# Performance work log

Measured on AMD Instinct MI355X. Metric: run time of the kernel, lower is better.

The kernel has to match this reference:

```python
import jax, jax.numpy as jnp
import numpy as np

B, T, D, H, F = 256, 128, 64, 512, 256


def setup_inputs() -> dict:
    key = jax.random.key(0)
    ks = jax.random.split(key, 4)
    return {
        "observations": jax.random.normal(ks[0], (B, T, D), dtype=jnp.float32),
        "Wx": jax.random.normal(ks[1], (D, 4 * H), dtype=jnp.float32) / np.sqrt(D),
        "Wh": jax.random.normal(ks[2], (H, 4 * H), dtype=jnp.float32) / np.sqrt(H),
        "b": jnp.zeros((4 * H,), dtype=jnp.float32),
        "Wd": jax.random.normal(ks[3], (H, F), dtype=jnp.float32) / np.sqrt(H),
        "bd": jnp.zeros((F,), dtype=jnp.float32),
    }


def reference(observations, Wx, Wh, b, Wd, bd):
    # observations: [B, T, D]. Flax nnx.LSTMCell gate order: i, f, g, o;
    # input kernels have no bias, hidden kernels carry the bias.
    batch = observations.shape[0]
    hidden = Wh.shape[0]
    # Precompute input projections for all timesteps in one big GEMM: [T, B, 4H]
    x_proj = jnp.einsum("btd,dg->tbg", observations, Wx)

    def step(carry, xp_t):
        c, h = carry
        gates = xp_t + h @ Wh + b  # [B, 4H]
        i, f, g, o = jnp.split(gates, 4, axis=-1)
        i = jax.nn.sigmoid(i)
        f = jax.nn.sigmoid(f)
        g = jnp.tanh(g)
        o = jax.nn.sigmoid(o)
        c_new = f * c + i * g
        h_new = o * jnp.tanh(c_new)
        return (c_new, h_new), None

    c0 = jnp.zeros((batch, hidden), dtype=observations.dtype)
    h0 = jnp.zeros((batch, hidden), dtype=observations.dtype)
    (c_last, h_last), _ = jax.lax.scan(step, (c0, h0), x_proj)
    return jax.nn.relu(h_last @ Wd + bd)
```

## Files before the change

### kernel.cpp

```cpp
#include <hip/hip_runtime.h>


#define WH_S 524
#define WX_S 72
#define HT_S 524

typedef __attribute__((ext_vector_type(4))) _Float16 f16x4;
typedef __attribute__((ext_vector_type(4))) float    f32x4;
typedef __attribute__((ext_vector_type(2))) unsigned long long u64x2;
typedef unsigned long long u64;

__device__ __forceinline__ float sigm(float x)  { return 1.f / (1.f + __expf(-x)); }
__device__ __forceinline__ float tanh_(float x) { float e = __expf(2.f * x); return 1.f - 2.f / (e + 1.f); }

__device__ __forceinline__ u64x2 ld128_cc(const void* p) {
    u64x2 v;
    asm volatile("global_load_dwordx4 %0, %1, off sc0 sc1" : "=v"(v) : "v"(p));
    return v;
}

#define MFMA16(w, a, c) __builtin_amdgcn_mfma_f32_16x16x16f16((w), (a), (c), 0, 0, 0)

__launch_bounds__(256, 1)
__global__ void lstm_persist(const float* __restrict__ obs,
                             const float* __restrict__ Wx,
                             const float* __restrict__ Wh,
                             const float* __restrict__ bvec,
                             u64* __restrict__ hbuf,
                             unsigned* __restrict__ bar)
{
    __shared__ _Float16 sbuf[128 * WH_S];

    const int tid = threadIdx.x, lane = tid & 63, wid = tid >> 6;
    const int grp = blockIdx.x & 15, slc = blockIdx.x >> 4;
    const int l15 = lane & 15, l16 = lane >> 4;
    const int c0 = (wid << 5) + l15, c1 = c0 + 16;

    for (int idx = tid; idx < 512 * 128; idx += 256) {
        int k = idx >> 7, c = idx & 127;
        int u = ((c >> 5) << 3) | (c & 7);
        int g = (((c >> 4) & 1) << 1) | ((c >> 3) & 1);
        sbuf[c * WH_S + k] = (_Float16)Wh[k * 2048 + (g << 9) + (slc << 5) + u];
    }
    __syncthreads();
    f16x4 wf0[32], wf1[32];
    #pragma unroll
    for (int kk = 0; kk < 32; ++kk) {
        wf0[kk] = *(const f16x4*)&sbuf[c0 * WH_S + (kk << 4) + (l16 << 2)];
        wf1[kk] = *(const f16x4*)&sbuf[c1 * WH_S + (kk << 4) + (l16 << 2)];
    }
    __syncthreads();
    for (int idx = tid; idx < 64 * 128; idx += 256) {
        int k = idx >> 7, c = idx & 127;
        int u = ((c >> 5) << 3) | (c & 7);
        int g = (((c >> 4) & 1) << 1) | ((c >> 3) & 1);
        sbuf[c * WX_S + k] = (_Float16)Wx[k * 2048 + (g << 9) + (slc << 5) + u];
    }
    __syncthreads();
    f16x4 xw0[4], xw1[4];
    #pragma unroll
    for (int kx = 0; kx < 4; ++kx) {
        xw0[kx] = *(const f16x4*)&sbuf[c0 * WX_S + (kx << 4) + (l16 << 2)];
        xw1[kx] = *(const f16x4*)&sbuf[c1 * WX_S + (kx << 4) + (l16 << 2)];
    }
    __syncthreads();
    _Float16* const sh = sbuf;

    const int brow = (grp << 4) + l15;
    const int ub   = (wid << 3) + ((l16 & 1) << 2);
    f32x4 bia[4];
    #pragma unroll
    for (int g = 0; g < 4; ++g)
        bia[g] = *(const f32x4*)(bvec + (g << 9) + (slc << 5) + ub);

    const int r_ld  = (wid << 2) + (lane >> 4);
    const int ch16  = lane & 15;
    const int hstore_idx = (brow << 7) + (slc << 3) + (wid << 1) + (l16 & 1);
    unsigned* const ctr = bar + (grp << 4);

    float c_reg[4] = {0.f, 0.f, 0.f, 0.f};

    for (int t = 0; t < 128; ++t) {
        const u64* hc = hbuf + ((t & 1) ? 32768 : 0);
        u64*       hn = hbuf + ((t & 1) ? 0 : 32768);

        const u64* hrow = hc + (((grp << 4) + r_ld) << 7) + (ch16 << 1);
        u64x2 hv4[4];
        #pragma unroll
        for (int j = 0; j < 4; ++j) hv4[j] = ld128_cc(hrow + (j << 5));

        f16x4 xf[4];
        const float* op = obs + ((brow << 7) + t) * 64;
        #pragma unroll
        for (int kx = 0; kx < 4; ++kx) {
            f32x4 ov = *(const f32x4*)(op + (kx << 4) + (l16 << 2));
            #pragma unroll
            for (int e = 0; e < 4; ++e) xf[kx][e] = (_Float16)ov[e];
        }

        asm volatile("s_waitcnt vmcnt(0)" ::: "memory");
        #pragma unroll
        for (int j = 0; j < 4; ++j) {
            *(u64*)&sh[r_ld * HT_S + (j << 7) + (ch16 << 3)]     = hv4[j][0];
            *(u64*)&sh[r_ld * HT_S + (j << 7) + (ch16 << 3) + 4] = hv4[j][1];
        }
        __syncthreads();

        f32x4 a00 = {0.f,0.f,0.f,0.f}, a01 = {0.f,0.f,0.f,0.f};
        f32x4 a10 = {0.f,0.f,0.f,0.f}, a11 = {0.f,0.f,0.f,0.f};

        #pragma unroll
        for (int kx = 0; kx < 4; ++kx) {
            if (kx & 1) { a01 = MFMA16(xw0[kx], xf[kx], a01); a11 = MFMA16(xw1[kx], xf[kx], a11); }
            else        { a00 = MFMA16(xw0[kx], xf[kx], a00); a10 = MFMA16(xw1[kx], xf[kx], a10); }
        }
        #pragma unroll
        for (int kk = 0; kk < 32; ++kk) {
            f16x4 af = *(const f16x4*)&sh[l15 * HT_S + (kk << 4) + (l16 << 2)];
            if (kk & 1) { a01 = MFMA16(wf0[kk], af, a01); a11 = MFMA16(wf1[kk], af, a11); }
            else        { a00 = MFMA16(wf0[kk], af, a00); a10 = MFMA16(wf1[kk], af, a10); }
        }
        f32x4 t0 = a00 + a01, t1 = a10 + a11;

        f32x4 r0, r1;
        #pragma unroll
        for (int rr = 0; rr < 4; ++rr) {
            r0[rr] = __shfl_xor(t0[rr], 32, 64);
            r1[rr] = __shfl_xor(t1[rr], 32, 64);
        }
        const bool low = (l16 < 2);
        f16x4 hv;
        #pragma unroll
        for (int rr = 0; rr < 4; ++rr) {
            float I  = low ? t0[rr] : r0[rr];
            float Fv = low ? r0[rr] : t0[rr];
            float G  = low ? t1[rr] : r1[rr];
            float O  = low ? r1[rr] : t1[rr];
            I  = sigm (I  + bia[0][rr]);
            Fv = sigm (Fv + bia[1][rr]);
            G  = tanh_(G  + bia[2][rr]);
            O  = sigm (O  + bia[3][rr]);
            float cn  = Fv * c_reg[rr] + I * G;
            c_reg[rr] = cn;
            hv[rr] = (_Float16)(O * tanh_(cn));
        }
        if (low)
            __hip_atomic_store(hn + hstore_idx, __builtin_bit_cast(u64, hv),
                               __ATOMIC_RELAXED, __HIP_MEMORY_SCOPE_AGENT);

        if (t < 127) {
            asm volatile("s_waitcnt vmcnt(0)" ::: "memory");
            __syncthreads();
            if (tid == 0) {
                __hip_atomic_fetch_add(ctr, 1u, __ATOMIC_RELAXED, __HIP_MEMORY_SCOPE_AGENT);
                const unsigned tgt = (unsigned)((t + 1) << 4);
                while (__hip_atomic_load(ctr, __ATOMIC_RELAXED, __HIP_MEMORY_SCOPE_AGENT) < tgt)
                    __builtin_amdgcn_s_sleep(1);
            }
            __syncthreads();
        }
    }
}

__launch_bounds__(256)
__global__ void final_proj(const _Float16* __restrict__ hlast,
                           const float* __restrict__ Wd,
                           const float* __restrict__ bd,
                           float* __restrict__ out)
{
    __shared__ float shm[2048];
    const int tid = threadIdx.x;
    const int rb  = blockIdx.x;
    for (int idx = tid; idx < 2048; idx += 256)
        shm[idx] = (float)hlast[(rb << 2) * 512 + idx];
    __syncthreads();
    float a0 = 0.f, a1 = 0.f, a2 = 0.f, a3 = 0.f;
    for (int k = 0; k < 512; ++k) {
        float w = Wd[(k << 8) + tid];
        a0 += shm[k] * w; a1 += shm[512 + k] * w; a2 += shm[1024 + k] * w; a3 += shm[1536 + k] * w;
    }
    float bb = bd[tid];
    float v0 = a0 + bb, v1 = a1 + bb, v2 = a2 + bb, v3 = a3 + bb;
    out[((rb << 2) + 0) * 256 + tid] = v0 > 0.f ? v0 : 0.f;
    out[((rb << 2) + 1) * 256 + tid] = v1 > 0.f ? v1 : 0.f;
    out[((rb << 2) + 2) * 256 + tid] = v2 > 0.f ? v2 : 0.f;
    out[((rb << 2) + 3) * 256 + tid] = v3 > 0.f ? v3 : 0.f;
}

extern "C" void kernel_launch(void* const* d_in, const int* in_sizes, int n_in,
                              void* d_out, int out_size, void* d_ws, size_t ws_size,
                              hipStream_t stream)
{
    (void)in_sizes; (void)n_in; (void)out_size; (void)ws_size;
    const float* obs = (const float*)d_in[0];
    const float* Wx  = (const float*)d_in[1];
    const float* Wh  = (const float*)d_in[2];
    const float* bv  = (const float*)d_in[3];
    const float* Wd  = (const float*)d_in[4];
    const float* bd  = (const float*)d_in[5];
    float* out = (float*)d_out;

    u64* hbuf     = (u64*)d_ws;
    unsigned* bar = (unsigned*)((char*)d_ws + 524288);

    hipMemsetAsync(d_ws, 0, 524288 + 1024, stream);

    void* args[6];
    args[0] = (void*)&obs; args[1] = (void*)&Wx; args[2] = (void*)&Wh;
    args[3] = (void*)&bv;  args[4] = (void*)&hbuf; args[5] = (void*)&bar;
    hipError_t e = hipLaunchCooperativeKernel((const void*)lstm_persist,
                                              dim3(256), dim3(256), args, 0, stream);
    if (e != hipSuccess) {
        lstm_persist<<<dim3(256), dim3(256), 0, stream>>>(obs, Wx, Wh, bv, hbuf, bar);
    }
    final_proj<<<dim3(64), dim3(256), 0, stream>>>((const _Float16*)d_ws, Wd, bd, out);
}
```

Measured before the change: 551.0 us.

## Replace per-group barrier counter with step-tagged hidden-state words polled by consumers

Drops the atomic counter barrier between timesteps. Each fp16 hidden value is now stored in a 32-bit word together with a 16-bit timestep tag, and consumers spin-load their rows until every tag matches the expected step. Blocks then wait only for the data they need instead of a full group arrive-and-wait, and one block-wide sync per step is removed. In exchange the hidden buffer doubles in size, so global traffic and the memset grow, and the design relies on each 128-bit store becoming visible as a unit.

```diff
diff --git a/kernel.cpp b/kernel.cpp
--- a/kernel.cpp
+++ b/kernel.cpp
@@ -7,16 +7,19 @@
 
 typedef __attribute__((ext_vector_type(4))) _Float16 f16x4;
 typedef __attribute__((ext_vector_type(4))) float    f32x4;
-typedef __attribute__((ext_vector_type(2))) unsigned long long u64x2;
-typedef unsigned long long u64;
+typedef __attribute__((ext_vector_type(4))) unsigned u32x4;
+typedef __attribute__((ext_vector_type(2))) unsigned u32x2;
 
 __device__ __forceinline__ float sigm(float x)  { return 1.f / (1.f + __expf(-x)); }
 __device__ __forceinline__ float tanh_(float x) { float e = __expf(2.f * x); return 1.f - 2.f / (e + 1.f); }
 
-__device__ __forceinline__ u64x2 ld128_cc(const void* p) {
-    u64x2 v;
+__device__ __forceinline__ u32x4 ldx4_cc(const unsigned* p) {
+    u32x4 v;
     asm volatile("global_load_dwordx4 %0, %1, off sc0 sc1" : "=v"(v) : "v"(p));
     return v;
+}
+__device__ __forceinline__ void stx4_cc(unsigned* p, u32x4 v) {
+    asm volatile("global_store_dwordx4 %0, %1, off sc0 sc1" :: "v"(p), "v"(v) : "memory");
 }
 
 #define MFMA16(w, a, c) __builtin_amdgcn_mfma_f32_16x16x16f16((w), (a), (c), 0, 0, 0)
@@ -26,8 +29,7 @@
                              const float* __restrict__ Wx,
                              const float* __restrict__ Wh,
                              const float* __restrict__ bvec,
-                             u64* __restrict__ hbuf,
-                             unsigned* __restrict__ bar)
+                             unsigned* __restrict__ hb)
 {
     __shared__ _Float16 sbuf[128 * WH_S];
 
@@ -73,22 +75,13 @@
     for (int g = 0; g < 4; ++g)
         bia[g] = *(const f32x4*)(bvec + (g << 9) + (slc << 5) + ub);
 
-    const int r_ld  = (wid << 2) + (lane >> 4);
-    const int ch16  = lane & 15;
-    const int hstore_idx = (brow << 7) + (slc << 3) + (wid << 1) + (l16 & 1);
-    unsigned* const ctr = bar + (grp << 4);
+    const int r_ld = (wid << 2) + l16;
+    const int ch16 = l15;
+    const int rowg = (grp << 4) + r_ld;
 
     float c_reg[4] = {0.f, 0.f, 0.f, 0.f};
 
     for (int t = 0; t < 128; ++t) {
-        const u64* hc = hbuf + ((t & 1) ? 32768 : 0);
-        u64*       hn = hbuf + ((t & 1) ? 0 : 32768);
-
-        const u64* hrow = hc + (((grp << 4) + r_ld) << 7) + (ch16 << 1);
-        u64x2 hv4[4];
-        #pragma unroll
-        for (int j = 0; j < 4; ++j) hv4[j] = ld128_cc(hrow + (j << 5));
-
         f16x4 xf[4];
         const float* op = obs + ((brow << 7) + t) * 64;
         #pragma unroll
@@ -97,18 +90,41 @@
             #pragma unroll
             for (int e = 0; e < 4; ++e) xf[kx][e] = (_Float16)ov[e];
         }
-
-        asm volatile("s_waitcnt vmcnt(0)" ::: "memory");
-        #pragma unroll
-        for (int j = 0; j < 4; ++j) {
-            *(u64*)&sh[r_ld * HT_S + (j << 7) + (ch16 << 3)]     = hv4[j][0];
-            *(u64*)&sh[r_ld * HT_S + (j << 7) + (ch16 << 3) + 4] = hv4[j][1];
+        __builtin_amdgcn_sched_barrier(0);
+
+        const unsigned tagt = (unsigned)t;
+        const unsigned* src = hb + ((t & 1) ? 131072 : 0) + rowg * 512 + (ch16 << 2);
+        u32x4 v[8];
+        #pragma unroll
+        for (int j = 0; j < 8; ++j) v[j] = ldx4_cc(src + (j << 6));
+        unsigned pend = 0xffu;
+        for (;;) {
+            asm volatile("s_waitcnt vmcnt(0)" ::: "memory");
+            unsigned np = 0;
+            #pragma unroll
+            for (int j = 0; j < 8; ++j) {
+                if (pend & (1u << j)) {
+                    bool ok = ((v[j][0] & 0xffffu) == tagt) & ((v[j][1] & 0xffffu) == tagt)
+                            & ((v[j][2] & 0xffffu) == tagt) & ((v[j][3] & 0xffffu) == tagt);
+                    if (!ok) { np |= (1u << j); v[j] = ldx4_cc(src + (j << 6)); }
+                }
+            }
+            pend = np;
+            if (!__any((int)pend)) break;
+        }
+        __builtin_amdgcn_sched_barrier(0);
+
+        #pragma unroll
+        for (int j = 0; j < 8; ++j) {
+            u32x2 wv;
+            wv[0] = __builtin_amdgcn_perm(v[j][1], v[j][0], 0x07060302);
+            wv[1] = __builtin_amdgcn_perm(v[j][3], v[j][2], 0x07060302);
+            *(u32x2*)&sh[r_ld * HT_S + (j << 6) + (ch16 << 2)] = wv;
         }
         __syncthreads();
 
         f32x4 a00 = {0.f,0.f,0.f,0.f}, a01 = {0.f,0.f,0.f,0.f};
         f32x4 a10 = {0.f,0.f,0.f,0.f}, a11 = {0.f,0.f,0.f,0.f};
-
         #pragma unroll
         for (int kx = 0; kx < 4; ++kx) {
             if (kx & 1) { a01 = MFMA16(xw0[kx], xf[kx], a01); a11 = MFMA16(xw1[kx], xf[kx], a11); }
@@ -144,26 +160,23 @@
             c_reg[rr] = cn;
             hv[rr] = (_Float16)(O * tanh_(cn));
         }
-        if (low)
-            __hip_atomic_store(hn + hstore_idx, __builtin_bit_cast(u64, hv),
-                               __ATOMIC_RELAXED, __HIP_MEMORY_SCOPE_AGENT);
-
-        if (t < 127) {
-            asm volatile("s_waitcnt vmcnt(0)" ::: "memory");
-            __syncthreads();
-            if (tid == 0) {
-                __hip_atomic_fetch_add(ctr, 1u, __ATOMIC_RELAXED, __HIP_MEMORY_SCOPE_AGENT);
-                const unsigned tgt = (unsigned)((t + 1) << 4);
-                while (__hip_atomic_load(ctr, __ATOMIC_RELAXED, __HIP_MEMORY_SCOPE_AGENT) < tgt)
-                    __builtin_amdgcn_s_sleep(1);
+        if (low) {
+            unsigned* dst = hb + (((t + 1) & 1) ? 131072 : 0)
+                          + (brow << 9) + (slc << 5) + (wid << 3) + ((l16 & 1) << 2);
+            u32x4 st;
+            #pragma unroll
+            for (int rr = 0; rr < 4; ++rr) {
+                unsigned short hbits = __builtin_bit_cast(unsigned short, (_Float16)hv[rr]);
+                st[rr] = (unsigned)(t + 1) | ((unsigned)hbits << 16);
             }
-            __syncthreads();
-        }
+            stx4_cc(dst, st);
+        }
+        __syncthreads();
     }
 }
 
 __launch_bounds__(256)
-__global__ void final_proj(const _Float16* __restrict__ hlast,
+__global__ void final_proj(const unsigned* __restrict__ hlast,
                            const float* __restrict__ Wd,
                            const float* __restrict__ bd,
                            float* __restrict__ out)
@@ -171,8 +184,10 @@
     __shared__ float shm[2048];
     const int tid = threadIdx.x;
     const int rb  = blockIdx.x;
-    for (int idx = tid; idx < 2048; idx += 256)
-        shm[idx] = (float)hlast[(rb << 2) * 512 + idx];
+    for (int idx = tid; idx < 2048; idx += 256) {
+        unsigned r = hlast[(rb << 2) * 512 + idx];
+        shm[idx] = (float)__builtin_bit_cast(_Float16, (unsigned short)(r >> 16));
+    }
     __syncthreads();
     float a0 = 0.f, a1 = 0.f, a2 = 0.f, a3 = 0.f;
     for (int k = 0; k < 512; ++k) {
@@ -200,18 +215,17 @@
     const float* bd  = (const float*)d_in[5];
     float* out = (float*)d_out;
 
-    u64* hbuf     = (u64*)d_ws;
-    unsigned* bar = (unsigned*)((char*)d_ws + 524288);
-
-    hipMemsetAsync(d_ws, 0, 524288 + 1024, stream);
-
-    void* args[6];
+    unsigned* hb = (unsigned*)d_ws;
+
+    hipMemsetAsync(d_ws, 0, 1048576, stream);
+
+    void* args[5];
     args[0] = (void*)&obs; args[1] = (void*)&Wx; args[2] = (void*)&Wh;
-    args[3] = (void*)&bv;  args[4] = (void*)&hbuf; args[5] = (void*)&bar;
+    args[3] = (void*)&bv;  args[4] = (void*)&hb;
     hipError_t e = hipLaunchCooperativeKernel((const void*)lstm_persist,
                                               dim3(256), dim3(256), args, 0, stream);
     if (e != hipSuccess) {
-        lstm_persist<<<dim3(256), dim3(256), 0, stream>>>(obs, Wx, Wh, bv, hbuf, bar);
-    }
-    final_proj<<<dim3(64), dim3(256), 0, stream>>>((const _Float16*)d_ws, Wd, bd, out);
-}
+        lstm_persist<<<dim3(256), dim3(256), 0, stream>>>(obs, Wx, Wh, bv, hb);
+    }
+    final_proj<<<dim3(64), dim3(256), 0, stream>>>(hb, Wd, bd, out);
+}
```

After: 643.9 us. +16.9%, slower.

## Replace atomic counter barrier with per-block step flags polled by one wavefront

Applied to the files above, without the earlier changes.

Each block in a 16-block group now stores its completed step index to its own flag slot. At the start of the next step, wavefront 0 polls all 16 group flags in parallel with cache-bypassing loads, which replaces the shared atomic counter and its single-thread spin. The wait also moves after the observation loads, so those loads overlap the synchronisation and the post-step syncthreads is dropped. This cuts atomic contention and one barrier per step. In exchange, correctness now depends on the ordering of the sc0/sc1 store and load between the h writes and the flag.

```diff
diff --git a/kernel.cpp b/kernel.cpp
--- a/kernel.cpp
+++ b/kernel.cpp
@@ -17,6 +17,15 @@
     u64x2 v;
     asm volatile("global_load_dwordx4 %0, %1, off sc0 sc1" : "=v"(v) : "v"(p));
     return v;
+}
+__device__ __forceinline__ unsigned ldflag_cc(const unsigned* p) {
+    unsigned v;
+    asm volatile("global_load_dword %0, %1, off sc0 sc1\n\ts_waitcnt vmcnt(0)"
+                 : "=v"(v) : "v"(p) : "memory");
+    return v;
+}
+__device__ __forceinline__ void stflag_cc(unsigned* p, unsigned v) {
+    asm volatile("global_store_dword %0, %1, off sc0 sc1" :: "v"(p), "v"(v) : "memory");
 }
 
 #define MFMA16(w, a, c) __builtin_amdgcn_mfma_f32_16x16x16f16((w), (a), (c), 0, 0, 0)
@@ -27,7 +36,7 @@
                              const float* __restrict__ Wh,
                              const float* __restrict__ bvec,
                              u64* __restrict__ hbuf,
-                             unsigned* __restrict__ bar)
+                             unsigned* __restrict__ flg)
 {
     __shared__ _Float16 sbuf[128 * WH_S];
 
@@ -73,21 +82,16 @@
     for (int g = 0; g < 4; ++g)
         bia[g] = *(const f32x4*)(bvec + (g << 9) + (slc << 5) + ub);
 
-    const int r_ld  = (wid << 2) + (lane >> 4);
-    const int ch16  = lane & 15;
+    const int r_ld  = (wid << 2) + l16;
+    const int ch16  = l15;
     const int hstore_idx = (brow << 7) + (slc << 3) + (wid << 1) + (l16 & 1);
-    unsigned* const ctr = bar + (grp << 4);
+    unsigned* const gflg = flg + (grp << 4);
 
     float c_reg[4] = {0.f, 0.f, 0.f, 0.f};
 
     for (int t = 0; t < 128; ++t) {
         const u64* hc = hbuf + ((t & 1) ? 32768 : 0);
         u64*       hn = hbuf + ((t & 1) ? 0 : 32768);
-
-        const u64* hrow = hc + (((grp << 4) + r_ld) << 7) + (ch16 << 1);
-        u64x2 hv4[4];
-        #pragma unroll
-        for (int j = 0; j < 4; ++j) hv4[j] = ld128_cc(hrow + (j << 5));
 
         f16x4 xf[4];
         const float* op = obs + ((brow << 7) + t) * 64;
@@ -97,7 +101,24 @@
             #pragma unroll
             for (int e = 0; e < 4; ++e) xf[kx][e] = (_Float16)ov[e];
         }
-
+        __builtin_amdgcn_sched_barrier(0);
+
+        if (t) {
+            if (wid == 0) {
+                const unsigned tgt = (unsigned)t;
+                for (;;) {
+                    unsigned f = ldflag_cc(gflg + l15);
+                    if (__all((int)(f >= tgt))) break;
+                    __builtin_amdgcn_s_sleep(1);
+                }
+            }
+            __syncthreads();
+        }
+
+        const u64* hrow = hc + (((grp << 4) + r_ld) << 7) + (ch16 << 1);
+        u64x2 hv4[4];
+        #pragma unroll
+        for (int j = 0; j < 4; ++j) hv4[j] = ld128_cc(hrow + (j << 5));
         asm volatile("s_waitcnt vmcnt(0)" ::: "memory");
         #pragma unroll
         for (int j = 0; j < 4; ++j) {
@@ -151,13 +172,8 @@
         if (t < 127) {
             asm volatile("s_waitcnt vmcnt(0)" ::: "memory");
             __syncthreads();
-            if (tid == 0) {
-                __hip_atomic_fetch_add(ctr, 1u, __ATOMIC_RELAXED, __HIP_MEMORY_SCOPE_AGENT);
-                const unsigned tgt = (unsigned)((t + 1) << 4);
-                while (__hip_atomic_load(ctr, __ATOMIC_RELAXED, __HIP_MEMORY_SCOPE_AGENT) < tgt)
-                    __builtin_amdgcn_s_sleep(1);
-            }
-            __syncthreads();
+            if (tid == 0)
+                stflag_cc(gflg + slc, (unsigned)(t + 1));
         }
     }
 }
@@ -201,17 +217,17 @@
     float* out = (float*)d_out;
 
     u64* hbuf     = (u64*)d_ws;
-    unsigned* bar = (unsigned*)((char*)d_ws + 524288);
+    unsigned* flg = (unsigned*)((char*)d_ws + 524288);
 
     hipMemsetAsync(d_ws, 0, 524288 + 1024, stream);
 
     void* args[6];
     args[0] = (void*)&obs; args[1] = (void*)&Wx; args[2] = (void*)&Wh;
-    args[3] = (void*)&bv;  args[4] = (void*)&hbuf; args[5] = (void*)&bar;
+    args[3] = (void*)&bv;  args[4] = (void*)&hbuf; args[5] = (void*)&flg;
     hipError_t e = hipLaunchCooperativeKernel((const void*)lstm_persist,
                                               dim3(256), dim3(256), args, 0, stream);
     if (e != hipSuccess) {
-        lstm_persist<<<dim3(256), dim3(256), 0, stream>>>(obs, Wx, Wh, bv, hbuf, bar);
+        lstm_persist<<<dim3(256), dim3(256), 0, stream>>>(obs, Wx, Wh, bv, hbuf, flg);
     }
     final_proj<<<dim3(64), dim3(256), 0, stream>>>((const _Float16*)d_ws, Wd, bd, out);
 }
```

Result: no change. 547.5 us (-0.6%).
